# Performance work log

Hardware: AMD Instinct MI355X
Metric: run time of the kernel (lower is better)

## Reference

```python
import jax, jax.numpy as jnp
import numpy as np

N_BANDS = 8
N_DIFF = 5
N_AVG = 11
N_GAUSS = 15
SIGMA_G = 3.0
A_LRELU = 0.0
EPS = 1e-8


def _lrelu(x, a=A_LRELU):
    return jnp.where(x >= 0, x, a * x)


def setup_inputs() -> dict:
    key = jax.random.key(0)
    k_x, k_b1, k_b2, k_b3 = jax.random.split(key, 4)
    B, F, T = 8, 512, 16384
    x = jax.random.uniform(k_x, (B, F, T), dtype=jnp.float32)

    # log-gamma compression parameter (per band)
    log_gamma = jnp.full((N_BANDS,), jnp.log(10.0), dtype=jnp.float32)

    # depthwise diff kernel along time: [-1, +1] centered
    dw = np.zeros((N_BANDS, 1, 1, N_DIFF), dtype=np.float32)
    dw[..., N_DIFF // 2] = -1.0
    dw[..., N_DIFF // 2 + 1] = 1.0
    diff_w = jnp.asarray(dw)
    diff_b = 0.01 * jax.random.normal(k_b1, (N_BANDS,), dtype=jnp.float32)

    # depthwise local-average conv1d
    avg_w = jnp.full((N_BANDS, 1, N_AVG), 1.0 / N_AVG, dtype=jnp.float32)
    avg_b = 0.01 * jax.random.normal(k_b2, (N_BANDS,), dtype=jnp.float32)

    mix_w = jnp.full((1, N_BANDS), 1.0 / N_BANDS, dtype=jnp.float32)

    # gaussian smoothing conv1d (note: original uses 2*sigma, not 2*sigma^2)
    n = np.arange(N_GAUSS, dtype=np.float32)
    gw = np.exp(-((n - N_GAUSS // 2) ** 2) / (2.0 * SIGMA_G)).astype(np.float32)
    gauss_w = jnp.asarray(gw).reshape(1, 1, N_GAUSS)
    gauss_b = 0.01 * jax.random.normal(k_b3, (1,), dtype=jnp.float32)

    return {"x": x, "log_gamma": log_gamma, "diff_w": diff_w, "diff_b": diff_b,
            "avg_w": avg_w, "avg_b": avg_b, "mix_w": mix_w,
            "gauss_w": gauss_w, "gauss_b": gauss_b}


def reference(x, log_gamma, diff_w, diff_b, avg_w, avg_b, mix_w, gauss_w, gauss_b):
    B, F, T = x.shape
    Fb = F // N_BANDS
    # chunk along freq into bands -> [B, C=N_bands, Fb, T] (matches permute in torch)
    xb = x.reshape(B, N_BANDS, Fb, T)
    # log-gamma compression (per-band gamma)
    gamma = jnp.exp(log_gamma)[None, :, None, None]
    x_log = jnp.log1p(gamma * xb)
    # depthwise temporal diff conv, 'same' padding
    x_diff = jax.lax.conv_general_dilated(
        x_log, diff_w, window_strides=(1, 1), padding='SAME',
        dimension_numbers=('NCHW', 'OIHW', 'NCHW'),
        feature_group_count=N_BANDS) + diff_b[None, :, None, None]
    # half-wave rectify, pool over frequency -> [B, C, T]
    x_pool = _lrelu(x_diff).sum(axis=2)
    # depthwise local average along time, subtract (enhancement)
    x_avg = jax.lax.conv_general_dilated(
        x_pool, avg_w, window_strides=(1,), padding='SAME',
        dimension_numbers=('NCH', 'OIH', 'NCH'),
        feature_group_count=N_BANDS) + avg_b[None, :, None]
    x_enh = x_pool - x_avg
    # mix bands: [B, C, T] x [1, C] -> [B, 1, T]
    x_mix = jnp.einsum('bct,oc->bot', x_enh, mix_w)
    # gaussian smoothing conv1d -> [B, T]
    x_gauss = (jax.lax.conv_general_dilated(
        x_mix, gauss_w, window_strides=(1,), padding='SAME',
        dimension_numbers=('NCH', 'OIH', 'NCH')) + gauss_b[None, :, None])[:, 0, :]
    # rectify and max-normalize
    x_act = _lrelu(x_gauss)
    x_act = x_act / (x_act.max(axis=1, keepdims=True) + EPS)
    return x_act
```

## Files before the change

kernel.cpp:

```cpp
#include <hip/hip_runtime.h>

#define TT 16384
#define BB 8
#define NB 8
#define FB 64
#define FSPLIT 4
#define FCHUNK (FB / FSPLIT)
#define TSM 256

__device__ __forceinline__ float lgf(float g, float x) {
    return __logf(fmaf(g, x, 1.0f));
}

__global__ __launch_bounds__(256) void pool_kernel(
    const float* __restrict__ x,
    const float* __restrict__ log_gamma,
    const float* __restrict__ diff_w,
    const float* __restrict__ diff_b,
    float* __restrict__ pool_part)
{
    const int bc = blockIdx.x;
    const int c  = bc & 7;
    const int t0 = blockIdx.y * 2048 + threadIdx.x * 8;
    const int f0 = blockIdx.z * FCHUNK;
    const float* __restrict__ xb = x + ((size_t)bc * FB + f0) * TT;

    const float g  = __expf(log_gamma[c]);
    const float w0 = diff_w[c * 5 + 0], w1 = diff_w[c * 5 + 1],
                w2 = diff_w[c * 5 + 2], w3 = diff_w[c * 5 + 3],
                w4 = diff_w[c * 5 + 4];
    const float bias = diff_b[c];

    const int b = min(max(t0 - 2, 0), TT - 12);
    const int s = t0 - 2 - b;
    const float* __restrict__ xr = xb + b;

    float acc[8] = {0.f,0.f,0.f,0.f,0.f,0.f,0.f,0.f};

    float4 p0 = *reinterpret_cast<const float4*>(xr);
    float4 p1 = *reinterpret_cast<const float4*>(xr + 4);
    float4 p2 = *reinterpret_cast<const float4*>(xr + 8);

    #pragma unroll 4
    for (int f = 0; f < FCHUNK; ++f) {
        const float4 c0 = p0, c1 = p1, c2 = p2;
        const float* __restrict__ nr = xr + (size_t)((f + 1 < FCHUNK) ? f + 1 : f) * TT;
        p0 = *reinterpret_cast<const float4*>(nr);
        p1 = *reinterpret_cast<const float4*>(nr + 4);
        p2 = *reinterpret_cast<const float4*>(nr + 8);

        float lg[12];
        lg[0]=lgf(g,c0.x); lg[1]=lgf(g,c0.y); lg[2] =lgf(g,c0.z); lg[3] =lgf(g,c0.w);
        lg[4]=lgf(g,c1.x); lg[5]=lgf(g,c1.y); lg[6] =lgf(g,c1.z); lg[7] =lgf(g,c1.w);
        lg[8]=lgf(g,c2.x); lg[9]=lgf(g,c2.y); lg[10]=lgf(g,c2.z); lg[11]=lgf(g,c2.w);

        float L[12];
        if (s == 0) {
            #pragma unroll
            for (int k = 0; k < 12; ++k) L[k] = lg[k];
        } else if (s < 0) {
            L[0] = 0.f; L[1] = 0.f;
            #pragma unroll
            for (int k = 2; k < 12; ++k) L[k] = lg[k - 2];
        } else {
            #pragma unroll
            for (int k = 0; k < 10; ++k) L[k] = lg[k + 2];
            L[10] = 0.f; L[11] = 0.f;
        }

        #pragma unroll
        for (int j = 0; j < 8; ++j) {
            const float d = fmaf(w0, L[j],
                            fmaf(w1, L[j + 1],
                            fmaf(w2, L[j + 2],
                            fmaf(w3, L[j + 3],
                            fmaf(w4, L[j + 4], bias)))));
            acc[j] += (d >= 0.f) ? d : 0.f;
        }
    }

    float* __restrict__ po = pool_part + ((size_t)blockIdx.z * (BB * NB) + bc) * TT + t0;
    *reinterpret_cast<float4*>(po)     = make_float4(acc[0], acc[1], acc[2], acc[3]);
    *reinterpret_cast<float4*>(po + 4) = make_float4(acc[4], acc[5], acc[6], acc[7]);
}

__global__ __launch_bounds__(256) void smooth_kernel(
    const float* __restrict__ pool_part,
    const float* __restrict__ avg_w,
    const float* __restrict__ avg_b,
    const float* __restrict__ mix_w,
    const float* __restrict__ gauss_w,
    const float* __restrict__ gauss_b,
    float* __restrict__ out,
    float* __restrict__ pmax)
{
    __shared__ float sp[NB][TSM + 24];
    __shared__ float sm[TSM + 14];
    __shared__ float wmax[4];

    const int b  = blockIdx.x >> 6;
    const int t0 = (blockIdx.x & 63) * TSM;

    for (int i = threadIdx.x; i < TSM + 24; i += 256) {
        const int t = t0 + i - 12;
        const bool in = ((unsigned)t < (unsigned)TT);
        const int tc = in ? t : (t < 0 ? 0 : TT - 1);
        #pragma unroll
        for (int c = 0; c < NB; ++c) {
            const size_t off = ((size_t)b * NB + c) * TT + tc;
            float s = 0.f;
            #pragma unroll
            for (int z = 0; z < FSPLIT; ++z)
                s += pool_part[(size_t)z * (BB * NB) * TT + off];
            sp[c][i] = in ? s : 0.f;
        }
    }
    __syncthreads();

    for (int i = threadIdx.x; i < TSM + 14; i += 256) {
        const int t = t0 + i - 7;
        float v = 0.f;
        if ((unsigned)t < (unsigned)TT) {
            #pragma unroll
            for (int c = 0; c < NB; ++c) {
                float av = 0.f;
                #pragma unroll
                for (int j = 0; j < 11; ++j)
                    av = fmaf(avg_w[c * 11 + j], sp[c][i + j], av);
                const float e = sp[c][i + 5] - av - avg_b[c];
                v = fmaf(mix_w[c], e, v);
            }
        }
        sm[i] = v;
    }
    __syncthreads();

    const int i = threadIdx.x;
    float gs = gauss_b[0];
    #pragma unroll
    for (int k = 0; k < 15; ++k)
        gs = fmaf(gauss_w[k], sm[i + k], gs);
    const float a = (gs >= 0.f) ? gs : 0.f;
    out[(size_t)b * TT + t0 + i] = a;

    float lmax = a;
    #pragma unroll
    for (int off = 32; off > 0; off >>= 1)
        lmax = fmaxf(lmax, __shfl_down(lmax, off, 64));
    if ((threadIdx.x & 63) == 0) wmax[threadIdx.x >> 6] = lmax;
    __syncthreads();
    if (threadIdx.x == 0)
        pmax[blockIdx.x] = fmaxf(fmaxf(wmax[0], wmax[1]), fmaxf(wmax[2], wmax[3]));
}

__global__ __launch_bounds__(256) void norm_kernel(
    float* __restrict__ out, const float* __restrict__ pmax)
{
    const int i = blockIdx.x * 256 + threadIdx.x;
    const int b = i >> 14;
    const float* __restrict__ pm = pmax + b * 64;
    float m = 0.f;
    #pragma unroll
    for (int k = 0; k < 64; ++k) m = fmaxf(m, pm[k]);
    out[i] = out[i] / (m + 1e-8f);
}

extern "C" void kernel_launch(void* const* d_in, const int* in_sizes, int n_in,
                              void* d_out, int out_size, void* d_ws, size_t ws_size,
                              hipStream_t stream) {
    const float* x        = (const float*)d_in[0];
    const float* log_g    = (const float*)d_in[1];
    const float* diff_w   = (const float*)d_in[2];
    const float* diff_b   = (const float*)d_in[3];
    const float* avg_w    = (const float*)d_in[4];
    const float* avg_b    = (const float*)d_in[5];
    const float* mix_w    = (const float*)d_in[6];
    const float* gauss_w  = (const float*)d_in[7];
    const float* gauss_b  = (const float*)d_in[8];
    float* out = (float*)d_out;

    float* pool_part = (float*)d_ws;
    float* pmax = (float*)((char*)d_ws + (size_t)FSPLIT * BB * NB * TT * sizeof(float));

    pool_kernel<<<dim3(BB * NB, TT / 2048, FSPLIT), 256, 0, stream>>>(
        x, log_g, diff_w, diff_b, pool_part);
    smooth_kernel<<<BB * (TT / TSM), 256, 0, stream>>>(pool_part, avg_w, avg_b, mix_w,
                                                       gauss_w, gauss_b, out, pmax);
    norm_kernel<<<(BB * TT) / 256, 256, 0, stream>>>(out, pmax);
}
```

Baseline: 387.1 us.

## Fuse frequency pooling with smoothing into one kernel using halo recompute

Merges the pool and smooth kernels into one. Each 320-thread block computes all 8 bands' frequency-pooled diffs for a 256-sample tile plus a 12-sample halo directly into shared memory, and each thread loops over all 64 frequency rows. This removes the partial-sum round trip through global memory and one kernel launch. In exchange the halo samples are recomputed (320 spans for 256 outputs), the frequency split that supplied parallelism is gone (512 blocks doing 64-row loops), and the edge handling is now per-element index clamping.

```diff
diff --git a/kernel.cpp b/kernel.cpp
--- a/kernel.cpp
+++ b/kernel.cpp
@@ -4,26 +4,38 @@
 #define BB 8
 #define NB 8
 #define FB 64
-#define FSPLIT 4
-#define FCHUNK (FB / FSPLIT)
 #define TSM 256
+#define NTHR 320
+#define SPANS 40
+#define SPC (SPANS * 8)
+#define HALO 12
 
 __device__ __forceinline__ float lgf(float g, float x) {
     return __logf(fmaf(g, x, 1.0f));
 }
 
-__global__ __launch_bounds__(256) void pool_kernel(
+__global__ __launch_bounds__(NTHR) void fused_kernel(
     const float* __restrict__ x,
     const float* __restrict__ log_gamma,
     const float* __restrict__ diff_w,
     const float* __restrict__ diff_b,
-    float* __restrict__ pool_part)
+    const float* __restrict__ avg_w,
+    const float* __restrict__ avg_b,
+    const float* __restrict__ mix_w,
+    const float* __restrict__ gauss_w,
+    const float* __restrict__ gauss_b,
+    float* __restrict__ out,
+    float* __restrict__ pmax)
 {
-    const int bc = blockIdx.x;
-    const int c  = bc & 7;
-    const int t0 = blockIdx.y * 2048 + threadIdx.x * 8;
-    const int f0 = blockIdx.z * FCHUNK;
-    const float* __restrict__ xb = x + ((size_t)bc * FB + f0) * TT;
+    __shared__ float sp[NB][SPC];
+    __shared__ float sm[TSM + 14];
+    __shared__ float wmax[NTHR / 64];
+
+    const int b   = blockIdx.x >> 6;
+    const int t0  = (blockIdx.x & 63) * TSM;
+    const int tid = threadIdx.x;
+    const int c    = tid / SPANS;
+    const int span = tid % SPANS;
 
     const float g  = __expf(log_gamma[c]);
     const float w0 = diff_w[c * 5 + 0], w1 = diff_w[c * 5 + 1],
@@ -31,9 +43,12 @@
                 w4 = diff_w[c * 5 + 4];
     const float bias = diff_b[c];
 
-    const int b = min(max(t0 - 2, 0), TT - 12);
-    const int s = t0 - 2 - b;
-    const float* __restrict__ xr = xb + b;
+    const int ts = t0 - HALO + span * 8;
+    const int  wb    = min(max(ts - 2, 0), TT - 12);
+    const int  delta = (ts - 2) - wb;
+    const bool edge  = (delta != 0) || (ts - 2 < 0) || (ts + 10 > TT);
+    const float* __restrict__ xr =
+        x + ((size_t)b * (NB * FB) + (size_t)c * FB) * TT + wb;
 
     float acc[8] = {0.f,0.f,0.f,0.f,0.f,0.f,0.f,0.f};
 
@@ -42,9 +57,9 @@
     float4 p2 = *reinterpret_cast<const float4*>(xr + 8);
 
     #pragma unroll 4
-    for (int f = 0; f < FCHUNK; ++f) {
+    for (int f = 0; f < FB; ++f) {
         const float4 c0 = p0, c1 = p1, c2 = p2;
-        const float* __restrict__ nr = xr + (size_t)((f + 1 < FCHUNK) ? f + 1 : f) * TT;
+        const float* __restrict__ nr = xr + (size_t)((f + 1 < FB) ? f + 1 : f) * TT;
         p0 = *reinterpret_cast<const float4*>(nr);
         p1 = *reinterpret_cast<const float4*>(nr + 4);
         p2 = *reinterpret_cast<const float4*>(nr + 8);
@@ -55,17 +70,16 @@
         lg[8]=lgf(g,c2.x); lg[9]=lgf(g,c2.y); lg[10]=lgf(g,c2.z); lg[11]=lgf(g,c2.w);
 
         float L[12];
-        if (s == 0) {
+        if (!edge) {
             #pragma unroll
             for (int k = 0; k < 12; ++k) L[k] = lg[k];
-        } else if (s < 0) {
-            L[0] = 0.f; L[1] = 0.f;
-            #pragma unroll
-            for (int k = 2; k < 12; ++k) L[k] = lg[k - 2];
         } else {
             #pragma unroll
-            for (int k = 0; k < 10; ++k) L[k] = lg[k + 2];
-            L[10] = 0.f; L[11] = 0.f;
+            for (int k = 0; k < 12; ++k) {
+                const int tk  = ts - 2 + k;
+                const int idx = min(max(k + delta, 0), 11);
+                L[k] = ((unsigned)tk < (unsigned)TT) ? lg[idx] : 0.f;
+            }
         }
 
         #pragma unroll
@@ -79,78 +93,55 @@
         }
     }
 
-    float* __restrict__ po = pool_part + ((size_t)blockIdx.z * (BB * NB) + bc) * TT + t0;
-    *reinterpret_cast<float4*>(po)     = make_float4(acc[0], acc[1], acc[2], acc[3]);
-    *reinterpret_cast<float4*>(po + 4) = make_float4(acc[4], acc[5], acc[6], acc[7]);
-}
-
-__global__ __launch_bounds__(256) void smooth_kernel(
-    const float* __restrict__ pool_part,
-    const float* __restrict__ avg_w,
-    const float* __restrict__ avg_b,
-    const float* __restrict__ mix_w,
-    const float* __restrict__ gauss_w,
-    const float* __restrict__ gauss_b,
-    float* __restrict__ out,
-    float* __restrict__ pmax)
-{
-    __shared__ float sp[NB][TSM + 24];
-    __shared__ float sm[TSM + 14];
-    __shared__ float wmax[4];
-
-    const int b  = blockIdx.x >> 6;
-    const int t0 = (blockIdx.x & 63) * TSM;
-
-    for (int i = threadIdx.x; i < TSM + 24; i += 256) {
-        const int t = t0 + i - 12;
-        const bool in = ((unsigned)t < (unsigned)TT);
-        const int tc = in ? t : (t < 0 ? 0 : TT - 1);
+    {
+        float* __restrict__ spc = &sp[c][span * 8];
         #pragma unroll
-        for (int c = 0; c < NB; ++c) {
-            const size_t off = ((size_t)b * NB + c) * TT + tc;
-            float s = 0.f;
-            #pragma unroll
-            for (int z = 0; z < FSPLIT; ++z)
-                s += pool_part[(size_t)z * (BB * NB) * TT + off];
-            sp[c][i] = in ? s : 0.f;
+        for (int q = 0; q < 8; ++q) {
+            const int t = ts + q;
+            spc[q] = ((unsigned)t < (unsigned)TT) ? acc[q] : 0.f;
         }
     }
     __syncthreads();
 
-    for (int i = threadIdx.x; i < TSM + 14; i += 256) {
-        const int t = t0 + i - 7;
+    if (tid < TSM + 14) {
+        const int t = t0 - 7 + tid;
         float v = 0.f;
         if ((unsigned)t < (unsigned)TT) {
             #pragma unroll
-            for (int c = 0; c < NB; ++c) {
+            for (int c2 = 0; c2 < NB; ++c2) {
                 float av = 0.f;
                 #pragma unroll
                 for (int j = 0; j < 11; ++j)
-                    av = fmaf(avg_w[c * 11 + j], sp[c][i + j], av);
-                const float e = sp[c][i + 5] - av - avg_b[c];
-                v = fmaf(mix_w[c], e, v);
+                    av = fmaf(avg_w[c2 * 11 + j], sp[c2][tid + j], av);
+                const float e = sp[c2][tid + 5] - av - avg_b[c2];
+                v = fmaf(mix_w[c2], e, v);
             }
         }
-        sm[i] = v;
+        sm[tid] = v;
     }
     __syncthreads();
 
-    const int i = threadIdx.x;
-    float gs = gauss_b[0];
-    #pragma unroll
-    for (int k = 0; k < 15; ++k)
-        gs = fmaf(gauss_w[k], sm[i + k], gs);
-    const float a = (gs >= 0.f) ? gs : 0.f;
-    out[(size_t)b * TT + t0 + i] = a;
-
-    float lmax = a;
+    float lmax = 0.f;
+    if (tid < TSM) {
+        float gs = gauss_b[0];
+        #pragma unroll
+        for (int k = 0; k < 15; ++k)
+            gs = fmaf(gauss_w[k], sm[tid + k], gs);
+        const float a = (gs >= 0.f) ? gs : 0.f;
+        out[(size_t)b * TT + t0 + tid] = a;
+        lmax = a;
+    }
     #pragma unroll
     for (int off = 32; off > 0; off >>= 1)
         lmax = fmaxf(lmax, __shfl_down(lmax, off, 64));
-    if ((threadIdx.x & 63) == 0) wmax[threadIdx.x >> 6] = lmax;
+    if ((tid & 63) == 0) wmax[tid >> 6] = lmax;
     __syncthreads();
-    if (threadIdx.x == 0)
-        pmax[blockIdx.x] = fmaxf(fmaxf(wmax[0], wmax[1]), fmaxf(wmax[2], wmax[3]));
+    if (tid == 0) {
+        float m = wmax[0];
+        #pragma unroll
+        for (int q = 1; q < NTHR / 64; ++q) m = fmaxf(m, wmax[q]);
+        pmax[blockIdx.x] = m;
+    }
 }
 
 __global__ __launch_bounds__(256) void norm_kernel(
@@ -179,12 +170,9 @@
     const float* gauss_b  = (const float*)d_in[8];
     float* out = (float*)d_out;
 
-    float* pool_part = (float*)d_ws;
-    float* pmax = (float*)((char*)d_ws + (size_t)FSPLIT * BB * NB * TT * sizeof(float));
+    float* pmax = (float*)d_ws;
 
-    pool_kernel<<<dim3(BB * NB, TT / 2048, FSPLIT), 256, 0, stream>>>(
-        x, log_g, diff_w, diff_b, pool_part);
-    smooth_kernel<<<BB * (TT / TSM), 256, 0, stream>>>(pool_part, avg_w, avg_b, mix_w,
-                                                       gauss_w, gauss_b, out, pmax);
+    fused_kernel<<<BB * (TT / TSM), NTHR, 0, stream>>>(
+        x, log_g, diff_w, diff_b, avg_w, avg_b, mix_w, gauss_w, gauss_b, out, pmax);
     norm_kernel<<<(BB * TT) / 256, 256, 0, stream>>>(out, pmax);
 }
```

Measured after the change: 435.9 us. 1.13x slower.
